# Optimization experiments

Measured on AMD Instinct MI355X. Metric: run time of the kernel, lower is better.

## Reference

```python
import jax, jax.numpy as jnp
import numpy as np

S = 4          # num_segments
T = 4096       # frames
D = 1024       # input_size == output_size
HEADS = 1
FREQ = 10000.0
DH = D // HEADS     # per-head width = 1024
TB = T // S         # block height = 1024
WB = DH // S        # block width  = 256


def _abs_pos(tb, d, freq):
    # Matches getAbsolutePosition: AP[p, 2i] = sin(p / freq^(2i/d)), AP[p, 2i+1] = cos(same).
    pos = jnp.arange(tb, dtype=jnp.float32)[:, None]          # [tb,1]
    i = jnp.arange(tb // 2, dtype=jnp.float32)[None, :]       # [1,tb//2]
    ang = pos / jnp.power(jnp.float32(freq), 2.0 * i / d)     # [tb,tb//2]
    ap = jnp.zeros((tb, tb), jnp.float32)
    return ap.at[:, 0::2].set(jnp.sin(ang)).at[:, 1::2].set(jnp.cos(ang))


def setup_inputs() -> dict:
    key = jax.random.key(0)
    ks = jax.random.split(key, 6)
    x = jax.random.normal(ks[0], (T, D), jnp.float32)
    Wq = jax.random.normal(ks[1], (HEADS, DH, D), jnp.float32) * 0.02
    Wk = jax.random.normal(ks[2], (HEADS, DH, D), jnp.float32) * 0.02
    Wv = jax.random.normal(ks[3], (HEADS, DH, D), jnp.float32) * 0.02
    Wout = jax.random.normal(ks[4], (D, D), jnp.float32) * 0.02
    Wout2 = jax.random.normal(ks[5], (WB, WB + 2), jnp.float32) * 0.05
    return {"x": x, "Wq": Wq, "Wk": Wk, "Wv": Wv, "Wout": Wout, "Wout2": Wout2}


def _forward(x, Wq, Wk, Wv, Wout, Wout2):
    # diversity = 1 - cosine similarity (F.normalize p=2 along dim=1)
    xu = x / jnp.maximum(jnp.linalg.norm(x, axis=1, keepdims=True), 1e-12)
    div = 1.0 - xu @ xu.T                                     # [T,T]

    Q = jnp.einsum('ti,hdi->htd', x, Wq)                      # [h,T,DH]
    K = jnp.einsum('ti,hdi->htd', x, Wk)
    V = jnp.einsum('ti,hdi->htd', x, Wv)

    def blk(A):  # [h,T,DH] -> [h,S*S,TB,WB], block (i,j) row-major as in local_x/local_y
        return A.reshape(-1, S, TB, S, WB).transpose(0, 1, 3, 2, 4).reshape(-1, S * S, TB, WB)

    qb, kb, vb = blk(Q), blk(K), blk(V)
    # diversity uses the diagonal row-block for every column-block j of row i
    drow = jnp.stack([div[i * TB:(i + 1) * TB, i * TB:(i + 1) * TB] for i in range(S)], 0)  # [S,TB,TB]
    db = jnp.repeat(drow, S, axis=0)[None]                    # [1,S*S,TB,TB]

    sim = jnp.einsum('hbqc,hbkc->hbqk', qb, kb) + _abs_pos(TB, D, FREQ)  # [h,S*S,TB,TB]
    attw = jax.nn.softmax(sim, axis=-1)
    # normalized row entropy, then L1-normalized (F.normalize p=1)
    ent = -(attw * jax.nn.log_softmax(sim, axis=-1)).sum(-1) / jnp.log(jnp.float32(TB))  # [h,S*S,TB]
    ent = ent / jnp.maximum(jnp.abs(ent).sum(-1, keepdims=True), 1e-12)

    dep = (db * attw).sum(-1) / db.sum(-1)                    # [h,S*S,TB]
    att_win = attw + dep[:, :, None, :] * attw                # dep_factor rows are identical
    ctx = jnp.einsum('hbqk,hbkc->hbqc', att_win, vb)          # [h,S*S,TB,WB]

    chars = jax.lax.stop_gradient(jnp.stack([ent, dep], axis=-1))  # [h,S*S,TB,2] (detach)
    y = jnp.concatenate([ctx, chars], axis=-1) @ Wout2.T      # [h,S*S,TB,WB]

    # reassemble grid of blocks back to [h,T,DH], concat heads, final projection
    y = y.reshape(-1, S, S, TB, WB).transpose(0, 1, 3, 2, 4).reshape(-1, T, DH)
    y = y.transpose(1, 0, 2).reshape(T, HEADS * DH)
    return y @ Wout.T                                         # [T,D]


def reference(x, Wq, Wk, Wv, Wout, Wout2):
    return _forward(x, Wq, Wk, Wv, Wout, Wout2)
```

## Files before the change

kernel.cpp:

```cpp
#include <hip/hip_runtime.h>
#include <hip/hip_bf16.h>

#define TT 4096
#define DD 1024
#define TBB 1024
#define WBB 256

typedef __attribute__((ext_vector_type(8))) _Float16 half8;
typedef __attribute__((ext_vector_type(4))) _Float16 half4;
typedef __attribute__((ext_vector_type(16))) float f32x16;

__device__ __forceinline__ unsigned short f2h(float v) {
  _Float16 h = (_Float16)v;
  return *reinterpret_cast<unsigned short*>(&h);
}
__device__ __forceinline__ float h2f(unsigned short u) {
  _Float16 h = *reinterpret_cast<_Float16*>(&u);
  return (float)h;
}

__device__ __forceinline__ void gl_lds16(const unsigned short* g, unsigned short* l) {
  __builtin_amdgcn_global_load_lds(
      (const __attribute__((address_space(1))) void*)(unsigned long long)(g),
      (__attribute__((address_space(3))) void*)(unsigned long long)(l),
      16, 0, 0);
}

__device__ __forceinline__ float waveSum(float v) {
#pragma unroll
  for (int o = 32; o > 0; o >>= 1) v += __shfl_down(v, o, 64);
  return v;
}
__device__ __forceinline__ float bSum(float v) {
#pragma unroll
  for (int o = 32; o > 0; o >>= 1) v += __shfl_xor(v, o, 64);
  return v;
}
__device__ __forceinline__ float bMax(float v) {
#pragma unroll
  for (int o = 32; o > 0; o >>= 1) v = fmaxf(v, __shfl_xor(v, o, 64));
  return v;
}

template <int EPI, typename OutT>
__global__ __launch_bounds__(256) void gemm_bt(
    const unsigned short* __restrict__ A, const unsigned short* __restrict__ B,
    OutT* __restrict__ C,
    int K, int lda, int ldb, int ldc,
    int zbase, int zdiv,
    long sAi, long sAj, long sBi, long sBj, long sCi, long sCj,
    long sAz, long sBz, long sCz,
    const float* __restrict__ e0, const float* __restrict__ e1,
    const float* __restrict__ e2, const float* __restrict__ e3)
{
  __shared__ __align__(16) unsigned short lA[2][4096];
  __shared__ __align__(16) unsigned short lB[2][4096];

  const int z = blockIdx.z, gz = zbase + z;
  const int zi = gz / zdiv, zj = gz - zi * zdiv;
  const unsigned short* Ab = A + (long)zi * sAi + (long)zj * sAj + (long)z * sAz;
  const unsigned short* Bb = B + (long)zi * sBi + (long)zj * sBj + (long)z * sBz;
  const long offC = (long)zi * sCi + (long)zj * sCj + (long)z * sCz;

  const int m0 = blockIdx.y * 128, n0 = blockIdx.x * 128;
  const int tid = threadIdx.x, wave = tid >> 6, lane = tid & 63;
  const int wm = (wave >> 1) * 64, wn = (wave & 1) * 64;
  const int srow = lane >> 2;
  const int scol = (((lane & 3) ^ ((srow >> 1) & 3))) * 8;
  const int l31 = lane & 31, khi = lane >> 5;
  const int sw2 = (l31 >> 1) & 3;

  f32x16 acc[2][2] = {};

  for (int k0 = 0; k0 < K; k0 += 64) {
#pragma unroll
    for (int h = 0; h < 2; ++h)
#pragma unroll
      for (int t = 0; t < 2; ++t) {
        const int r = wave * 32 + t * 16 + srow;
        gl_lds16(Ab + (long)(m0 + r) * lda + (k0 + h * 32 + scol), &lA[h][wave * 1024 + t * 512]);
        gl_lds16(Bb + (long)(n0 + r) * ldb + (k0 + h * 32 + scol), &lB[h][wave * 1024 + t * 512]);
      }
    __syncthreads();

    half8 af[2][4], bfr[2][4];
#pragma unroll
    for (int mi = 0; mi < 2; ++mi)
#pragma unroll
      for (int ks = 0; ks < 4; ++ks)
        af[mi][ks] = *(const half8*)&lA[ks >> 1][(wm + mi * 32 + l31) * 32 + ((((ks & 1) * 2 + khi) ^ sw2) * 8)];
#pragma unroll
    for (int ni = 0; ni < 2; ++ni)
#pragma unroll
      for (int ks = 0; ks < 4; ++ks)
        bfr[ni][ks] = *(const half8*)&lB[ks >> 1][(wn + ni * 32 + l31) * 32 + ((((ks & 1) * 2 + khi) ^ sw2) * 8)];

#pragma unroll
    for (int ks = 0; ks < 4; ++ks)
#pragma unroll
      for (int mi = 0; mi < 2; ++mi)
#pragma unroll
        for (int ni = 0; ni < 2; ++ni)
          acc[mi][ni] = __builtin_amdgcn_mfma_f32_32x32x16_f16(af[mi][ks], bfr[ni][ks], acc[mi][ni], 0, 0, 0);
    __syncthreads();
  }

  OutT* Cb = C + offC;
#pragma unroll
  for (int mi = 0; mi < 2; ++mi)
#pragma unroll
    for (int ni = 0; ni < 2; ++ni)
#pragma unroll
      for (int r = 0; r < 16; ++r) {
        const int row = m0 + wm + mi * 32 + khi * 4 + (r & 3) + 8 * (r >> 2);
        const int col = n0 + wn + ni * 32 + l31;
        float v = acc[mi][ni][r];
        const long ci = (long)row * ldc + col;
        if constexpr (sizeof(OutT) == 2) {
          Cb[ci] = (OutT)f2h(v);
        } else {
          Cb[ci] = v;
        }
      }
}

template <int EPI, typename OutT>
__global__ __launch_bounds__(256) void gemm_s(
    const unsigned short* __restrict__ A, const unsigned short* __restrict__ B,
    OutT* __restrict__ C,
    int K, int lda, int ldb, int ldc,
    int zbase, int zdiv,
    long sAi, long sAj, long sBi, long sBj, long sCi, long sCj,
    long sAz, long sBz, long sCz,
    const float* __restrict__ e0, const float* __restrict__ e1,
    const float* __restrict__ e2, const float* __restrict__ e3)
{
  __shared__ __align__(16) unsigned short lA[2][2048];
  __shared__ __align__(16) unsigned short lB[2][2048];

  if constexpr (EPI == 2) {
    if (blockIdx.x < blockIdx.y) return;
  }

  const int z = blockIdx.z, gz = zbase + z;
  const int zi = gz / zdiv, zj = gz - zi * zdiv;
  const unsigned short* Ab = A + (long)zi * sAi + (long)zj * sAj + (long)z * sAz;
  const unsigned short* Bb = B + (long)zi * sBi + (long)zj * sBj + (long)z * sBz;
  const long offC = (long)zi * sCi + (long)zj * sCj + (long)z * sCz;

  const int m0 = blockIdx.y * 64, n0 = blockIdx.x * 64;
  const int tid = threadIdx.x, wave = tid >> 6, lane = tid & 63;
  const int wm = (wave >> 1) * 32, wn = (wave & 1) * 32;
  const int srow = lane >> 2;
  const int grow = wave * 16 + srow;
  const int scol = (((lane & 3) ^ ((grow >> 1) & 3))) * 8;
  const int l31 = lane & 31, khi = lane >> 5;
  const int sw2 = (l31 >> 1) & 3;

  f32x16 acc = {};

  for (int k0 = 0; k0 < K; k0 += 64) {
#pragma unroll
    for (int h = 0; h < 2; ++h) {
      gl_lds16(Ab + (long)(m0 + grow) * lda + (k0 + h * 32 + scol), &lA[h][wave * 512]);
      gl_lds16(Bb + (long)(n0 + grow) * ldb + (k0 + h * 32 + scol), &lB[h][wave * 512]);
    }
    __syncthreads();

    half8 af[4], bfr[4];
#pragma unroll
    for (int ks = 0; ks < 4; ++ks) {
      af[ks] = *(const half8*)&lA[ks >> 1][(wm + l31) * 32 + ((((ks & 1) * 2 + khi) ^ sw2) * 8)];
      bfr[ks] = *(const half8*)&lB[ks >> 1][(wn + l31) * 32 + ((((ks & 1) * 2 + khi) ^ sw2) * 8)];
    }
#pragma unroll
    for (int ks = 0; ks < 4; ++ks)
      acc = __builtin_amdgcn_mfma_f32_32x32x16_f16(af[ks], bfr[ks], acc, 0, 0, 0);
    __syncthreads();
  }

  OutT* Cb = C + offC;
  float Ef[4], Df[4];
  if constexpr (EPI == 4) {
    const int col0 = n0 + wn + l31;
#pragma unroll
    for (int j = 0; j < 4; ++j) {
      Ef[j] = e2[j * 1024 + col0];
      Df[j] = e3[j * 1024 + col0];
    }
  }
#pragma unroll
  for (int r = 0; r < 16; ++r) {
    const int row = m0 + wm + khi * 4 + (r & 3) + 8 * (r >> 2);
    const int col = n0 + wn + l31;
    float v = acc[r];
    if constexpr (EPI == 1 || EPI == 2) v = 1.0f - v;
    if constexpr (EPI == 4) {
      const float4 en = *(const float4*)(e0 + (long)row * 4);
      const float4 dp = *(const float4*)(e1 + (long)row * 4);
      v += en.x * Ef[0] + en.y * Ef[1] + en.z * Ef[2] + en.w * Ef[3]
         + dp.x * Df[0] + dp.y * Df[1] + dp.z * Df[2] + dp.w * Df[3];
    }
    const long ci = (long)row * ldc + col;
    if constexpr (sizeof(OutT) == 2) {
      Cb[ci] = (OutT)f2h(v);
    } else {
      Cb[ci] = v;
    }
  }

  if constexpr (EPI == 2) {
    if (blockIdx.x != blockIdx.y) {
      unsigned short* mir = &lA[0][0];
      const int lc = wn + l31;
#pragma unroll
      for (int chunk = 0; chunk < 2; ++chunk) {
        __syncthreads();
        if ((lc >> 5) == chunk) {
#pragma unroll
          for (int r = 0; r < 16; ++r) {
            const int lr = wm + khi * 4 + (r & 3) + 8 * (r >> 2);
            mir[(lc & 31) * 68 + lr] = f2h(1.0f - acc[r]);
          }
        }
        __syncthreads();
        const int cl = tid >> 3, co = (tid & 7) * 8;
        const ushort4 a = *(const ushort4*)&mir[cl * 68 + co];
        const ushort4 b = *(const ushort4*)&mir[cl * 68 + co + 4];
        unsigned short* dst = (unsigned short*)Cb + (long)(n0 + chunk * 32 + cl) * ldc + m0 + co;
        *(ushort4*)dst = a;
        *(ushort4*)(dst + 4) = b;
      }
    }
  }
}

__global__ __launch_bounds__(256) void sim_gemm(
    const unsigned short* __restrict__ A, const unsigned short* __restrict__ B,
    unsigned short* __restrict__ C,
    const unsigned short* __restrict__ APh)
{
  __shared__ __align__(16) unsigned short lA[2][4096];
  __shared__ __align__(16) unsigned short lB[2][4096];

  const int gz = blockIdx.z;
  const int zi = gz >> 2, zj = gz & 3;
  const unsigned short* Ab = A + (long)zi * (TBB * DD) + zj * WBB;
  const unsigned short* Bb = B + (long)zi * (TBB * DD) + zj * WBB;
  unsigned short* Cb = C + (long)gz * TBB * TBB;

  const int m0 = blockIdx.y * 128, n0 = blockIdx.x * 128;
  const int tid = threadIdx.x, wave = tid >> 6, lane = tid & 63;
  const int wm = (wave >> 1) * 64, wn = (wave & 1) * 64;
  const int srow = lane >> 2;
  const int scol = ((lane & 3) ^ ((srow >> 1) & 3)) * 8;
  const int l31 = lane & 31, khi = lane >> 5;
  const int sw2 = (l31 >> 1) & 3;

  f32x16 acc[2][2] = {};

  for (int k0 = 0; k0 < WBB; k0 += 64) {
#pragma unroll
    for (int h = 0; h < 2; ++h)
#pragma unroll
      for (int t = 0; t < 2; ++t) {
        const int r = wave * 32 + t * 16 + srow;
        gl_lds16(Ab + (long)(m0 + r) * DD + (k0 + h * 32 + scol), &lA[h][wave * 1024 + t * 512]);
        gl_lds16(Bb + (long)(n0 + r) * DD + (k0 + h * 32 + scol), &lB[h][wave * 1024 + t * 512]);
      }
    __syncthreads();

    half8 af[2][4], bfr[2][4];
#pragma unroll
    for (int mi = 0; mi < 2; ++mi)
#pragma unroll
      for (int ks = 0; ks < 4; ++ks)
        af[mi][ks] = *(const half8*)&lA[ks >> 1][(wm + mi * 32 + l31) * 32 + ((((ks & 1) * 2 + khi) ^ sw2) * 8)];
#pragma unroll
    for (int ni = 0; ni < 2; ++ni)
#pragma unroll
      for (int ks = 0; ks < 4; ++ks)
        bfr[ni][ks] = *(const half8*)&lB[ks >> 1][(wn + ni * 32 + l31) * 32 + ((((ks & 1) * 2 + khi) ^ sw2) * 8)];

#pragma unroll
    for (int ks = 0; ks < 4; ++ks)
#pragma unroll
      for (int mi = 0; mi < 2; ++mi)
#pragma unroll
        for (int ni = 0; ni < 2; ++ni)
          acc[mi][ni] = __builtin_amdgcn_mfma_f32_32x32x16_f16(af[mi][ks], bfr[ni][ks], acc[mi][ni], 0, 0, 0);
    __syncthreads();
  }

#pragma unroll
  for (int mi = 0; mi < 2; ++mi)
#pragma unroll
    for (int ni = 0; ni < 2; ++ni)
#pragma unroll
      for (int r = 0; r < 16; ++r) {
        const int row = m0 + wm + mi * 32 + khi * 4 + (r & 3) + 8 * (r >> 2);
        const int col = n0 + wn + ni * 32 + l31;
        Cb[(long)row * TBB + col] = f2h(acc[mi][ni][r] + h2f(APh[(long)row * 1024 + col]));
      }
}

__global__ __launch_bounds__(256) void ctx_gemm_s(
    const unsigned short* __restrict__ simh, const float* __restrict__ dep2,
    const float* __restrict__ Brow,
    const unsigned short* __restrict__ Vt, unsigned short* __restrict__ ctxR)
{
  __shared__ __align__(16) unsigned short lA[2][2048];
  __shared__ __align__(16) unsigned short lB[2][2048];
  __shared__ __align__(16) unsigned short sDepH[1024];

  const int gz = blockIdx.z, zi = gz >> 2, zj = gz & 3;
  const int m0 = blockIdx.y * 64, n0 = blockIdx.x * 64;
  const int tid = threadIdx.x, wave = tid >> 6, lane = tid & 63;
  const int wm = (wave >> 1) * 32, wn = (wave & 1) * 32;
  const int srow = lane >> 2;
  const int grow = wave * 16 + srow;
  const int scol = ((lane & 3) ^ ((grow >> 1) & 3)) * 8;
  const int l31 = lane & 31, khi = lane >> 5;
  const int sw2 = (l31 >> 1) & 3;

#pragma unroll
  for (int p = 0; p < 4; ++p)
    sDepH[tid + p * 256] =
        f2h(1.f + dep2[((long)zi * 1024 + tid + p * 256) * 4 + zj]);
  __syncthreads();

  const float B0 = Brow[(long)gz * 1024 + m0 + (tid >> 3)];
  const float B1 = Brow[(long)gz * 1024 + m0 + 32 + (tid >> 3)];

  const unsigned short* Ab = simh + (long)gz * TBB * TBB;
  const unsigned short* Bb = Vt + (long)(zj * 256) * TT + (long)zi * 1024;

  f32x16 acc = {};

  for (int k0 = 0; k0 < 1024; k0 += 64) {
#pragma unroll
    for (int h = 0; h < 2; ++h)
      gl_lds16(Bb + (long)(n0 + grow) * TT + (k0 + h * 32 + scol), &lB[h][wave * 512]);
#pragma unroll
    for (int h = 0; h < 2; ++h)
#pragma unroll
      for (int p = 0; p < 2; ++p) {
        const int idx = p * 1024 + tid * 4;
        const int row = idx >> 5, col = idx & 31;
        const ushort4 wv = *(const ushort4*)(Ab + (long)(m0 + row) * 1024 + k0 + h * 32 + col);
        const float Bp = p ? B1 : B0;
        half4 ev;
        ev.x = (_Float16)exp2f(fmaf(h2f(wv.x), 1.4426950408889634f, -Bp));
        ev.y = (_Float16)exp2f(fmaf(h2f(wv.y), 1.4426950408889634f, -Bp));
        ev.z = (_Float16)exp2f(fmaf(h2f(wv.z), 1.4426950408889634f, -Bp));
        ev.w = (_Float16)exp2f(fmaf(h2f(wv.w), 1.4426950408889634f, -Bp));
        const half4 dv = *(const half4*)&sDepH[k0 + h * 32 + col];
        half4 pv = ev * dv;
        const int pcol = (((col >> 3) ^ ((row >> 1) & 3)) << 3) | (col & 7);
        *(half4*)&lA[h][row * 32 + pcol] = pv;
      }
    __syncthreads();

    half8 af[4], bfr[4];
#pragma unroll
    for (int ks = 0; ks < 4; ++ks) {
      af[ks] = *(const half8*)&lA[ks >> 1][(wm + l31) * 32 + ((((ks & 1) * 2 + khi) ^ sw2) * 8)];
      bfr[ks] = *(const half8*)&lB[ks >> 1][(wn + l31) * 32 + ((((ks & 1) * 2 + khi) ^ sw2) * 8)];
    }
#pragma unroll
    for (int ks = 0; ks < 4; ++ks)
      acc = __builtin_amdgcn_mfma_f32_32x32x16_f16(af[ks], bfr[ks], acc, 0, 0, 0);
    __syncthreads();
  }

#pragma unroll
  for (int r = 0; r < 16; ++r) {
    const int row = m0 + wm + khi * 4 + (r & 3) + 8 * (r >> 2);
    const int col = n0 + wn + l31;
    ctxR[((long)zi * 1024 + row) * 1024 + zj * 256 + col] = f2h(acc[r]);
  }
}

__global__ __launch_bounds__(256) void prepx_kernel(
    const float* __restrict__ x, unsigned short* __restrict__ xh,
    unsigned short* __restrict__ xu)
{
  const int t = blockIdx.x, tid = threadIdx.x;
  const float4 v = *((const float4*)(x + (long)t * DD) + tid);
  float ss = v.x * v.x + v.y * v.y + v.z * v.z + v.w * v.w;
  ss = waveSum(ss);
  __shared__ float red[4];
  if ((tid & 63) == 0) red[tid >> 6] = ss;
  __syncthreads();
  const float tot = red[0] + red[1] + red[2] + red[3];
  const float inv = 1.f / fmaxf(sqrtf(tot), 1e-12f);
  ushort4 h, u;
  h.x = f2h(v.x); h.y = f2h(v.y); h.z = f2h(v.z); h.w = f2h(v.w);
  u.x = f2h(v.x * inv); u.y = f2h(v.y * inv); u.z = f2h(v.z * inv); u.w = f2h(v.w * inv);
  *((ushort4*)(xh + (long)t * DD) + tid) = h;
  *((ushort4*)(xu + (long)t * DD) + tid) = u;
}

__global__ __launch_bounds__(256) void castall_kernel(
    const float* __restrict__ Wq, const float* __restrict__ Wk,
    const float* __restrict__ Wv, const float* __restrict__ Wo,
    unsigned short* __restrict__ Wh, unsigned short* __restrict__ WoB)
{
  const long idx4 = ((long)blockIdx.x * 256 + threadIdx.x) * 4;
  const int which = (int)(idx4 >> 20);
  const long loc = idx4 & ((1L << 20) - 1);
  const float* src = (which == 0) ? Wq : ((which == 1) ? Wk : ((which == 2) ? Wv : Wo));
  unsigned short* dst = (which < 3) ? (Wh + idx4) : (WoB + loc);
  const float4 v = *(const float4*)(src + loc);
  ushort4 h;
  h.x = f2h(v.x); h.y = f2h(v.y); h.z = f2h(v.z); h.w = f2h(v.w);
  *(ushort4*)dst = h;
}

__global__ __launch_bounds__(256) void packw2_kernel(
    const float* __restrict__ W2, unsigned short* __restrict__ W2T,
    float* __restrict__ Ecol, float* __restrict__ Dcol)
{
  const int w = blockIdx.x, c = threadIdx.x;
  W2T[c * 256 + w] = f2h(W2[w * 258 + c]);
  if (c == 0) {
    Ecol[w] = W2[w * 258 + 256];
    Dcol[w] = W2[w * 258 + 257];
  }
}

__global__ __launch_bounds__(256) void ap_kernel(unsigned short* __restrict__ APh)
{
  const int p = blockIdx.x, tid = threadIdx.x;
#pragma unroll
  for (int t = 0; t < 2; ++t) {
    const int pr = tid + t * 256;
    const float e = (float)pr * (1.0f / 512.0f);
    const float ang = (float)p * exp2f(e * -13.287712379549449f);
    float s, c;
    sincosf(ang, &s, &c);
    ushort2 o;
    o.x = f2h(s); o.y = f2h(c);
    *(ushort2*)(APh + (long)p * 1024 + 2 * pr) = o;
  }
}

__global__ __launch_bounds__(256) void stats_kernel(
    const unsigned short* __restrict__ sim, const unsigned short* __restrict__ divb,
    float* __restrict__ dep2, float* __restrict__ ent2,
    float* __restrict__ Brow)
{
  const int gz = blockIdx.y, bi = gz >> 2;
  const int wave = threadIdx.x >> 6, lane = threadIdx.x & 63;
  const int q = blockIdx.x * 4 + wave;
  const unsigned short* srow = sim + ((long)gz * TBB + q) * TBB;
  const unsigned short* drow = divb + ((long)bi * TBB + q) * TBB;
  float s[16], d[16];
#pragma unroll
  for (int u = 0; u < 4; ++u) {
    const ushort4 sv = *(const ushort4*)(srow + u * 256 + lane * 4);
    const ushort4 dv = *(const ushort4*)(drow + u * 256 + lane * 4);
    s[u * 4 + 0] = h2f(sv.x); s[u * 4 + 1] = h2f(sv.y);
    s[u * 4 + 2] = h2f(sv.z); s[u * 4 + 3] = h2f(sv.w);
    d[u * 4 + 0] = h2f(dv.x); d[u * 4 + 1] = h2f(dv.y);
    d[u * 4 + 2] = h2f(dv.z); d[u * 4 + 3] = h2f(dv.w);
  }
  float m = s[0];
#pragma unroll
  for (int i = 1; i < 16; ++i) m = fmaxf(m, s[i]);
  m = bMax(m);
  const float mB = m * 1.4426950408889634f;
  float l = 0.f, ss = 0.f, dn = 0.f, ds = 0.f;
#pragma unroll
  for (int i = 0; i < 16; ++i) {
    const float e = exp2f(fmaf(s[i], 1.4426950408889634f, -mB));
    l += e; ss += e * s[i]; dn += e * d[i]; ds += d[i];
  }
  l = bSum(l); ss = bSum(ss); dn = bSum(dn); ds = bSum(ds);
  if (lane == 0) {
    const float Li = 1.f / l;
    const float lnL = logf(l);
    const long o2 = ((long)bi * 1024 + q) * 4 + (gz & 3);
    dep2[o2] = (dn * Li) / ds;
    ent2[o2] = (m + lnL - ss * Li) * 0.14426950408889634f;
    Brow[(long)gz * TBB + q] = (m + lnL) * 1.4426950408889634f;
  }
}

__global__ __launch_bounds__(256) void prefinal_kernel(
    float* __restrict__ ent2, const float* __restrict__ Ecol,
    const float* __restrict__ Dcol, const float* __restrict__ Wo,
    float* __restrict__ Efold, float* __restrict__ Dfold)
{
  const int b = blockIdx.x, tid = threadIdx.x;
  if (b < 4) {
    float4 v[4];
    float4 a = {0.f, 0.f, 0.f, 0.f};
#pragma unroll
    for (int p = 0; p < 4; ++p) {
      v[p] = *(const float4*)(ent2 + ((long)b * 1024 + tid + p * 256) * 4);
      a.x += fabsf(v[p].x); a.y += fabsf(v[p].y);
      a.z += fabsf(v[p].z); a.w += fabsf(v[p].w);
    }
    a.x = waveSum(a.x); a.y = waveSum(a.y);
    a.z = waveSum(a.z); a.w = waveSum(a.w);
    __shared__ float red[4][4];
    if ((tid & 63) == 0) {
      const int w = tid >> 6;
      red[w][0] = a.x; red[w][1] = a.y; red[w][2] = a.z; red[w][3] = a.w;
    }
    __syncthreads();
    float4 sc;
    sc.x = 1.f / fmaxf(red[0][0] + red[1][0] + red[2][0] + red[3][0], 1e-12f);
    sc.y = 1.f / fmaxf(red[0][1] + red[1][1] + red[2][1] + red[3][1], 1e-12f);
    sc.z = 1.f / fmaxf(red[0][2] + red[1][2] + red[2][2] + red[3][2], 1e-12f);
    sc.w = 1.f / fmaxf(red[0][3] + red[1][3] + red[2][3] + red[3][3], 1e-12f);
#pragma unroll
    for (int p = 0; p < 4; ++p) {
      float4 o = v[p];
      o.x *= sc.x; o.y *= sc.y; o.z *= sc.z; o.w *= sc.w;
      *(float4*)(ent2 + ((long)b * 1024 + tid + p * 256) * 4) = o;
    }
  } else {
    const int idx = (b - 4) * 256 + tid;
    const int j = idx >> 10, d = idx & 1023;
    const float* wrow = Wo + (long)d * 1024 + j * 256;
    float se = 0.f, sd = 0.f;
    for (int w = 0; w < 256; ++w) {
      const float wv = wrow[w];
      se += Ecol[w] * wv;
      sd += Dcol[w] * wv;
    }
    Efold[j * 1024 + d] = se;
    Dfold[j * 1024 + d] = sd;
  }
}

extern "C" void kernel_launch(void* const* d_in, const int* in_sizes, int n_in,
                              void* d_out, int out_size, void* d_ws, size_t ws_size,
                              hipStream_t stream)
{
  const float* x  = (const float*)d_in[0];
  const float* Wq = (const float*)d_in[1];
  const float* Wk = (const float*)d_in[2];
  const float* Wv = (const float*)d_in[3];
  const float* Wo = (const float*)d_in[4];
  const float* W2 = (const float*)d_in[5];

  char* ws = (char*)d_ws;
  size_t off = 0;
  auto take = [&](size_t bytes) -> void* {
    void* p = ws + off;
    off += (bytes + 255) & ~(size_t)255;
    return p;
  };
  unsigned short* QKV = (unsigned short*)take((size_t)2 * TT * DD * 2);
  unsigned short* xh  = (unsigned short*)take((size_t)TT * DD * 2);
  unsigned short* xu  = (unsigned short*)take((size_t)TT * DD * 2);
  unsigned short* Wh  = (unsigned short*)take((size_t)3 * DD * DD * 2);
  unsigned short* WoB = (unsigned short*)take((size_t)DD * DD * 2);
  unsigned short* W2T = (unsigned short*)take((size_t)256 * 256 * 2);
  unsigned short* WFh = (unsigned short*)take((size_t)DD * DD * 2);
  float* Ecol = (float*)take(256 * 4);
  float* Dcol = (float*)take(256 * 4);
  float* Efold = (float*)take((size_t)4 * DD * 4);
  float* Dfold = (float*)take((size_t)4 * DD * 4);
  unsigned short* APh = (unsigned short*)take((size_t)TBB * TBB * 2);
  unsigned short* divb = (unsigned short*)take((size_t)4 * TBB * TBB * 2);
  unsigned short* Vt = (unsigned short*)take((size_t)DD * TT * 2);
  unsigned short* simh = (unsigned short*)take((size_t)16 * TBB * TBB * 2);
  float* dep2 = (float*)take((size_t)TT * 4 * 4);
  float* ent2 = (float*)take((size_t)TT * 4 * 4);
  float* Brow = (float*)take((size_t)16 * TBB * 4);
  unsigned short* ctxR = (unsigned short*)take((size_t)TT * DD * 2);
  (void)ws_size; (void)in_sizes; (void)n_in; (void)out_size;

  prepx_kernel<<<TT, 256, 0, stream>>>(x, xh, xu);
  castall_kernel<<<(4 * DD * DD) / 1024, 256, 0, stream>>>(Wq, Wk, Wv, Wo, Wh, WoB);
  packw2_kernel<<<256, 256, 0, stream>>>(W2, W2T, Ecol, Dcol);
  ap_kernel<<<TBB, 256, 0, stream>>>(APh);

  gemm_s<0, unsigned short><<<dim3(4, 16, 4), 256, 0, stream>>>(
      WoB, W2T, WFh,
      256, DD, 256, DD, 0, 4,
      0, 256, 0, 0, 0, 256,
      0, 0, 0, nullptr, nullptr, nullptr, nullptr);

  gemm_bt<0, unsigned short><<<dim3(DD / 128, TT / 128, 2), 256, 0, stream>>>(
      xh, Wh, QKV,
      DD, DD, DD, DD, 0, 1,
      0, 0, (long)DD * DD, 0, (long)TT * DD, 0,
      0, 0, 0, nullptr, nullptr, nullptr, nullptr);

  gemm_s<0, unsigned short><<<dim3(TT / 64, DD / 64, 1), 256, 0, stream>>>(
      Wh + (size_t)2 * DD * DD, xh, Vt,
      DD, DD, DD, TT, 0, 1,
      0, 0, 0, 0, 0, 0,
      0, 0, 0, nullptr, nullptr, nullptr, nullptr);

  gemm_s<2, unsigned short><<<dim3(16, 16, 4), 256, 0, stream>>>(
      xu, xu, divb,
      DD, DD, DD, TBB, 0, 1,
      (long)TBB * DD, 0, (long)TBB * DD, 0, (long)TBB * TBB, 0,
      0, 0, 0, nullptr, nullptr, nullptr, nullptr);

  const unsigned short* Qh = QKV;
  const unsigned short* Kh = QKV + (size_t)TT * DD;

  sim_gemm<<<dim3(8, 8, 16), 256, 0, stream>>>(Qh, Kh, simh, APh);

  stats_kernel<<<dim3(TBB / 4, 16), 256, 0, stream>>>(simh, divb, dep2, ent2, Brow);

  prefinal_kernel<<<20, 256, 0, stream>>>(ent2, Ecol, Dcol, Wo, Efold, Dfold);

  ctx_gemm_s<<<dim3(4, 16, 16), 256, 0, stream>>>(simh, dep2, Brow, Vt, ctxR);

  gemm_s<4, float><<<dim3(16, 64, 1), 256, 0, stream>>>(
      ctxR, WFh, (float*)d_out,
      DD, DD, DD, DD, 0, 1,
      0, 0, 0, 0, 0, 0,
      0, 0, 0, ent2, dep2, Efold, Dfold);
}
```

Measured before the change: 255.4 us.

## Merge prep kernels, fold ent normalization into ctx GEMM, widen ctx tile

```diff
diff --git a/kernel.cpp b/kernel.cpp
--- a/kernel.cpp
+++ b/kernel.cpp
@@ -307,16 +307,52 @@
 __global__ __launch_bounds__(256) void ctx_gemm_s(
     const unsigned short* __restrict__ simh, const float* __restrict__ dep2,
     const float* __restrict__ Brow,
-    const unsigned short* __restrict__ Vt, unsigned short* __restrict__ ctxR)
+    const unsigned short* __restrict__ Vt, unsigned short* __restrict__ ctxR,
+    float* __restrict__ ent2)
 {
+  const int tid = threadIdx.x;
+
+  if (blockIdx.y == 16) {
+    if (blockIdx.x != 0 || blockIdx.z >= 4) return;
+    const int b = blockIdx.z;
+    float4 v[4];
+    float4 a = {0.f, 0.f, 0.f, 0.f};
+#pragma unroll
+    for (int p = 0; p < 4; ++p) {
+      v[p] = *(const float4*)(ent2 + ((long)b * 1024 + tid + p * 256) * 4);
+      a.x += fabsf(v[p].x); a.y += fabsf(v[p].y);
+      a.z += fabsf(v[p].z); a.w += fabsf(v[p].w);
+    }
+    a.x = waveSum(a.x); a.y = waveSum(a.y);
+    a.z = waveSum(a.z); a.w = waveSum(a.w);
+    __shared__ float red[4][4];
+    if ((tid & 63) == 0) {
+      const int w = tid >> 6;
+      red[w][0] = a.x; red[w][1] = a.y; red[w][2] = a.z; red[w][3] = a.w;
+    }
+    __syncthreads();
+    float4 sc;
+    sc.x = 1.f / fmaxf(red[0][0] + red[1][0] + red[2][0] + red[3][0], 1e-12f);
+    sc.y = 1.f / fmaxf(red[0][1] + red[1][1] + red[2][1] + red[3][1], 1e-12f);
+    sc.z = 1.f / fmaxf(red[0][2] + red[1][2] + red[2][2] + red[3][2], 1e-12f);
+    sc.w = 1.f / fmaxf(red[0][3] + red[1][3] + red[2][3] + red[3][3], 1e-12f);
+#pragma unroll
+    for (int p = 0; p < 4; ++p) {
+      float4 o = v[p];
+      o.x *= sc.x; o.y *= sc.y; o.z *= sc.z; o.w *= sc.w;
+      *(float4*)(ent2 + ((long)b * 1024 + tid + p * 256) * 4) = o;
+    }
+    return;
+  }
+
   __shared__ __align__(16) unsigned short lA[2][2048];
-  __shared__ __align__(16) unsigned short lB[2][2048];
+  __shared__ __align__(16) unsigned short lB[2][4096];
   __shared__ __align__(16) unsigned short sDepH[1024];
 
   const int gz = blockIdx.z, zi = gz >> 2, zj = gz & 3;
-  const int m0 = blockIdx.y * 64, n0 = blockIdx.x * 64;
-  const int tid = threadIdx.x, wave = tid >> 6, lane = tid & 63;
-  const int wm = (wave >> 1) * 32, wn = (wave & 1) * 32;
+  const int m0 = blockIdx.y * 64, n0 = blockIdx.x * 128;
+  const int wave = tid >> 6, lane = tid & 63;
+  const int wm = (wave >> 1) * 32, wn0 = (wave & 1) * 64;
   const int srow = lane >> 2;
   const int grow = wave * 16 + srow;
   const int scol = ((lane & 3) ^ ((grow >> 1) & 3)) * 8;
@@ -335,12 +371,14 @@
   const unsigned short* Ab = simh + (long)gz * TBB * TBB;
   const unsigned short* Bb = Vt + (long)(zj * 256) * TT + (long)zi * 1024;
 
-  f32x16 acc = {};
+  f32x16 acc[2] = {};
 
   for (int k0 = 0; k0 < 1024; k0 += 64) {
 #pragma unroll
-    for (int h = 0; h < 2; ++h)
+    for (int h = 0; h < 2; ++h) {
       gl_lds16(Bb + (long)(n0 + grow) * TT + (k0 + h * 32 + scol), &lB[h][wave * 512]);
+      gl_lds16(Bb + (long)(n0 + 64 + grow) * TT + (k0 + h * 32 + scol), &lB[h][2048 + wave * 512]);
+    }
 #pragma unroll
     for (int h = 0; h < 2; ++h)
 #pragma unroll
@@ -361,87 +399,121 @@
       }
     __syncthreads();
 
-    half8 af[4], bfr[4];
+    half8 af[4], bfr[2][4];
 #pragma unroll
     for (int ks = 0; ks < 4; ++ks) {
       af[ks] = *(const half8*)&lA[ks >> 1][(wm + l31) * 32 + ((((ks & 1) * 2 + khi) ^ sw2) * 8)];
-      bfr[ks] = *(const half8*)&lB[ks >> 1][(wn + l31) * 32 + ((((ks & 1) * 2 + khi) ^ sw2) * 8)];
+#pragma unroll
+      for (int n = 0; n < 2; ++n)
+        bfr[n][ks] = *(const half8*)&lB[ks >> 1][(wn0 + n * 32 + l31) * 32 + ((((ks & 1) * 2 + khi) ^ sw2) * 8)];
     }
 #pragma unroll
     for (int ks = 0; ks < 4; ++ks)
-      acc = __builtin_amdgcn_mfma_f32_32x32x16_f16(af[ks], bfr[ks], acc, 0, 0, 0);
-    __syncthreads();
-  }
-
-#pragma unroll
-  for (int r = 0; r < 16; ++r) {
-    const int row = m0 + wm + khi * 4 + (r & 3) + 8 * (r >> 2);
-    const int col = n0 + wn + l31;
-    ctxR[((long)zi * 1024 + row) * 1024 + zj * 256 + col] = f2h(acc[r]);
-  }
-}
-
-__global__ __launch_bounds__(256) void prepx_kernel(
-    const float* __restrict__ x, unsigned short* __restrict__ xh,
-    unsigned short* __restrict__ xu)
+#pragma unroll
+      for (int n = 0; n < 2; ++n)
+        acc[n] = __builtin_amdgcn_mfma_f32_32x32x16_f16(af[ks], bfr[n][ks], acc[n], 0, 0, 0);
+    __syncthreads();
+  }
+
+#pragma unroll
+  for (int n = 0; n < 2; ++n)
+#pragma unroll
+    for (int r = 0; r < 16; ++r) {
+      const int row = m0 + wm + khi * 4 + (r & 3) + 8 * (r >> 2);
+      const int col = n0 + wn0 + n * 32 + l31;
+      ctxR[((long)zi * 1024 + row) * 1024 + zj * 256 + col] = f2h(acc[n][r]);
+    }
+}
+
+__global__ __launch_bounds__(256) void prep_kernel(
+    const float* __restrict__ x, const float* __restrict__ Wq,
+    const float* __restrict__ Wk, const float* __restrict__ Wv,
+    const float* __restrict__ Wo, const float* __restrict__ W2,
+    unsigned short* __restrict__ xh, unsigned short* __restrict__ xu,
+    unsigned short* __restrict__ Wh, unsigned short* __restrict__ APh,
+    unsigned short* __restrict__ WFh, float* __restrict__ Efold,
+    float* __restrict__ Dfold)
 {
-  const int t = blockIdx.x, tid = threadIdx.x;
-  const float4 v = *((const float4*)(x + (long)t * DD) + tid);
-  float ss = v.x * v.x + v.y * v.y + v.z * v.z + v.w * v.w;
-  ss = waveSum(ss);
   __shared__ float red[4];
-  if ((tid & 63) == 0) red[tid >> 6] = ss;
-  __syncthreads();
-  const float tot = red[0] + red[1] + red[2] + red[3];
-  const float inv = 1.f / fmaxf(sqrtf(tot), 1e-12f);
-  ushort4 h, u;
-  h.x = f2h(v.x); h.y = f2h(v.y); h.z = f2h(v.z); h.w = f2h(v.w);
-  u.x = f2h(v.x * inv); u.y = f2h(v.y * inv); u.z = f2h(v.z * inv); u.w = f2h(v.w * inv);
-  *((ushort4*)(xh + (long)t * DD) + tid) = h;
-  *((ushort4*)(xu + (long)t * DD) + tid) = u;
-}
-
-__global__ __launch_bounds__(256) void castall_kernel(
-    const float* __restrict__ Wq, const float* __restrict__ Wk,
-    const float* __restrict__ Wv, const float* __restrict__ Wo,
-    unsigned short* __restrict__ Wh, unsigned short* __restrict__ WoB)
-{
-  const long idx4 = ((long)blockIdx.x * 256 + threadIdx.x) * 4;
-  const int which = (int)(idx4 >> 20);
-  const long loc = idx4 & ((1L << 20) - 1);
-  const float* src = (which == 0) ? Wq : ((which == 1) ? Wk : ((which == 2) ? Wv : Wo));
-  unsigned short* dst = (which < 3) ? (Wh + idx4) : (WoB + loc);
-  const float4 v = *(const float4*)(src + loc);
-  ushort4 h;
-  h.x = f2h(v.x); h.y = f2h(v.y); h.z = f2h(v.z); h.w = f2h(v.w);
-  *(ushort4*)dst = h;
-}
-
-__global__ __launch_bounds__(256) void packw2_kernel(
-    const float* __restrict__ W2, unsigned short* __restrict__ W2T,
-    float* __restrict__ Ecol, float* __restrict__ Dcol)
-{
-  const int w = blockIdx.x, c = threadIdx.x;
-  W2T[c * 256 + w] = f2h(W2[w * 258 + c]);
-  if (c == 0) {
-    Ecol[w] = W2[w * 258 + 256];
-    Dcol[w] = W2[w * 258 + 257];
-  }
-}
-
-__global__ __launch_bounds__(256) void ap_kernel(unsigned short* __restrict__ APh)
-{
-  const int p = blockIdx.x, tid = threadIdx.x;
-#pragma unroll
-  for (int t = 0; t < 2; ++t) {
-    const int pr = tid + t * 256;
-    const float e = (float)pr * (1.0f / 512.0f);
-    const float ang = (float)p * exp2f(e * -13.287712379549449f);
-    float s, c;
-    sincosf(ang, &s, &c);
-    ushort2 o;
-    o.x = f2h(s); o.y = f2h(c);
-    *(ushort2*)(APh + (long)p * 1024 + 2 * pr) = o;
+  int b = blockIdx.x;
+  const int tid = threadIdx.x;
+
+  if (b < 4096) {
+    const int t = b;
+    const float4 v = *((const float4*)(x + (long)t * DD) + tid);
+    float ss = v.x * v.x + v.y * v.y + v.z * v.z + v.w * v.w;
+    ss = waveSum(ss);
+    if ((tid & 63) == 0) red[tid >> 6] = ss;
+    __syncthreads();
+    const float tot = red[0] + red[1] + red[2] + red[3];
+    const float inv = 1.f / fmaxf(sqrtf(tot), 1e-12f);
+    ushort4 h, u;
+    h.x = f2h(v.x); h.y = f2h(v.y); h.z = f2h(v.z); h.w = f2h(v.w);
+    u.x = f2h(v.x * inv); u.y = f2h(v.y * inv); u.z = f2h(v.z * inv); u.w = f2h(v.w * inv);
+    *((ushort4*)(xh + (long)t * DD) + tid) = h;
+    *((ushort4*)(xu + (long)t * DD) + tid) = u;
+    return;
+  }
+  b -= 4096;
+  if (b < 3072) {
+    const long idx4 = ((long)b * 256 + tid) * 4;
+    const int which = (int)(idx4 >> 20);
+    const long loc = idx4 & ((1L << 20) - 1);
+    const float* src = (which == 0) ? Wq : ((which == 1) ? Wk : Wv);
+    const float4 v = *(const float4*)(src + loc);
+    ushort4 h;
+    h.x = f2h(v.x); h.y = f2h(v.y); h.z = f2h(v.z); h.w = f2h(v.w);
+    *(ushort4*)(Wh + idx4) = h;
+    return;
+  }
+  b -= 3072;
+  if (b < 1024) {
+    const int p = b;
+#pragma unroll
+    for (int t = 0; t < 2; ++t) {
+      const int pr = tid + t * 256;
+      const float e = (float)pr * (1.0f / 512.0f);
+      const float ang = (float)p * exp2f(e * -13.287712379549449f);
+      float s, c;
+      sincosf(ang, &s, &c);
+      ushort2 o;
+      o.x = f2h(s); o.y = f2h(c);
+      *(ushort2*)(APh + (long)p * 1024 + 2 * pr) = o;
+    }
+    return;
+  }
+  b -= 1024;
+  if (b < 256) {
+    const int d0 = b * 4;
+    float acc[4][4] = {};
+    for (int w = 0; w < 256; ++w) {
+      const float w2v = W2[w * 258 + tid];
+#pragma unroll
+      for (int dd = 0; dd < 4; ++dd)
+#pragma unroll
+        for (int j = 0; j < 4; ++j)
+          acc[dd][j] += Wo[(long)(d0 + dd) * 1024 + j * 256 + w] * w2v;
+    }
+#pragma unroll
+    for (int dd = 0; dd < 4; ++dd)
+#pragma unroll
+      for (int j = 0; j < 4; ++j)
+        WFh[(long)(d0 + dd) * 1024 + j * 256 + tid] = f2h(acc[dd][j]);
+    return;
+  }
+  b -= 256;
+  {
+    const int idx = b * 256 + tid;
+    const int j = idx >> 10, d = idx & 1023;
+    const float* wrow = Wo + (long)d * 1024 + j * 256;
+    float se = 0.f, sd = 0.f;
+    for (int w = 0; w < 256; ++w) {
+      const float wv = wrow[w];
+      se += W2[w * 258 + 256] * wv;
+      sd += W2[w * 258 + 257] * wv;
+    }
+    Efold[j * 1024 + d] = se;
+    Dfold[j * 1024 + d] = sd;
   }
 }
 
@@ -487,55 +559,6 @@
   }
 }
 
-__global__ __launch_bounds__(256) void prefinal_kernel(
-    float* __restrict__ ent2, const float* __restrict__ Ecol,
-    const float* __restrict__ Dcol, const float* __restrict__ Wo,
-    float* __restrict__ Efold, float* __restrict__ Dfold)
-{
-  const int b = blockIdx.x, tid = threadIdx.x;
-  if (b < 4) {
-    float4 v[4];
-    float4 a = {0.f, 0.f, 0.f, 0.f};
-#pragma unroll
-    for (int p = 0; p < 4; ++p) {
-      v[p] = *(const float4*)(ent2 + ((long)b * 1024 + tid + p * 256) * 4);
-      a.x += fabsf(v[p].x); a.y += fabsf(v[p].y);
-      a.z += fabsf(v[p].z); a.w += fabsf(v[p].w);
-    }
-    a.x = waveSum(a.x); a.y = waveSum(a.y);
-    a.z = waveSum(a.z); a.w = waveSum(a.w);
-    __shared__ float red[4][4];
-    if ((tid & 63) == 0) {
-      const int w = tid >> 6;
-      red[w][0] = a.x; red[w][1] = a.y; red[w][2] = a.z; red[w][3] = a.w;
-    }
-    __syncthreads();
-    float4 sc;
-    sc.x = 1.f / fmaxf(red[0][0] + red[1][0] + red[2][0] + red[3][0], 1e-12f);
-    sc.y = 1.f / fmaxf(red[0][1] + red[1][1] + red[2][1] + red[3][1], 1e-12f);
-    sc.z = 1.f / fmaxf(red[0][2] + red[1][2] + red[2][2] + red[3][2], 1e-12f);
-    sc.w = 1.f / fmaxf(red[0][3] + red[1][3] + red[2][3] + red[3][3], 1e-12f);
-#pragma unroll
-    for (int p = 0; p < 4; ++p) {
-      float4 o = v[p];
-      o.x *= sc.x; o.y *= sc.y; o.z *= sc.z; o.w *= sc.w;
-      *(float4*)(ent2 + ((long)b * 1024 + tid + p * 256) * 4) = o;
-    }
-  } else {
-    const int idx = (b - 4) * 256 + tid;
-    const int j = idx >> 10, d = idx & 1023;
-    const float* wrow = Wo + (long)d * 1024 + j * 256;
-    float se = 0.f, sd = 0.f;
-    for (int w = 0; w < 256; ++w) {
-      const float wv = wrow[w];
-      se += Ecol[w] * wv;
-      sd += Dcol[w] * wv;
-    }
-    Efold[j * 1024 + d] = se;
-    Dfold[j * 1024 + d] = sd;
-  }
-}
-
 extern "C" void kernel_launch(void* const* d_in, const int* in_sizes, int n_in,
                               void* d_out, int out_size, void* d_ws, size_t ws_size,
                               hipStream_t stream)
@@ -558,11 +581,7 @@
   unsigned short* xh  = (unsigned short*)take((size_t)TT * DD * 2);
   unsigned short* xu  = (unsigned short*)take((size_t)TT * DD * 2);
   unsigned short* Wh  = (unsigned short*)take((size_t)3 * DD * DD * 2);
-  unsigned short* WoB = (unsigned short*)take((size_t)DD * DD * 2);
-  unsigned short* W2T = (unsigned short*)take((size_t)256 * 256 * 2);
   unsigned short* WFh = (unsigned short*)take((size_t)DD * DD * 2);
-  float* Ecol = (float*)take(256 * 4);
-  float* Dcol = (float*)take(256 * 4);
   float* Efold = (float*)take((size_t)4 * DD * 4);
   float* Dfold = (float*)take((size_t)4 * DD * 4);
   unsigned short* APh = (unsigned short*)take((size_t)TBB * TBB * 2);
@@ -575,16 +594,8 @@
   unsigned short* ctxR = (unsigned short*)take((size_t)TT * DD * 2);
   (void)ws_size; (void)in_sizes; (void)n_in; (void)out_size;
 
-  prepx_kernel<<<TT, 256, 0, stream>>>(x, xh, xu);
-  castall_kernel<<<(4 * DD * DD) / 1024, 256, 0, stream>>>(Wq, Wk, Wv, Wo, Wh, WoB);
-  packw2_kernel<<<256, 256, 0, stream>>>(W2, W2T, Ecol, Dcol);
-  ap_kernel<<<TBB, 256, 0, stream>>>(APh);
-
-  gemm_s<0, unsigned short><<<dim3(4, 16, 4), 256, 0, stream>>>(
-      WoB, W2T, WFh,
-      256, DD, 256, DD, 0, 4,
-      0, 256, 0, 0, 0, 256,
-      0, 0, 0, nullptr, nullptr, nullptr, nullptr);
+  prep_kernel<<<8464, 256, 0, stream>>>(x, Wq, Wk, Wv, Wo, W2,
+                                        xh, xu, Wh, APh, WFh, Efold, Dfold);
 
   gemm_bt<0, unsigned short><<<dim3(DD / 128, TT / 128, 2), 256, 0, stream>>>(
       xh, Wh, QKV,
@@ -611,9 +622,7 @@
 
   stats_kernel<<<dim3(TBB / 4, 16), 256, 0, stream>>>(simh, divb, dep2, ent2, Brow);
 
-  prefinal_kernel<<<20, 256, 0, stream>>>(ent2, Ecol, Dcol, Wo, Efold, Dfold);
-
-  ctx_gemm_s<<<dim3(4, 16, 16), 256, 0, stream>>>(simh, dep2, Brow, Vt, ctxR);
+  ctx_gemm_s<<<dim3(2, 17, 16), 256, 0, stream>>>(simh, dep2, Brow, Vt, ctxR, ent2);
 
   gemm_s<4, float><<<dim3(16, 64, 1), 256, 0, stream>>>(
       ctxR, WFh, (float*)d_out,
```

Result: slower. 280.8 us (+9.9%).
